# Kernel optimization log

Hardware: AMD Instinct MI355X
Metric: run time of the kernel (lower is better)

## Reference

```python
import jax, jax.numpy as jnp
import numpy as np

H = 256   # hidden_dim
S = 16    # d_state
B = 2
N = 8192
LN_EPS = 1e-5


def setup_inputs() -> dict:
    key = jax.random.key(0)
    ks = jax.random.split(key, 12)
    std = 1.0 / np.sqrt(H)
    inp = {
        'x': jax.random.normal(ks[0], (B, N, H), dtype=jnp.float32),
        'in_w': jax.random.normal(ks[1], (2 * H, H), dtype=jnp.float32) * std,
        'in_b': jax.random.normal(ks[2], (2 * H,), dtype=jnp.float32) * std,
        'xp_w': jax.random.normal(ks[3], (2 * S + 1, H), dtype=jnp.float32) * std,
        'xp_b': jax.random.normal(ks[4], (2 * S + 1,), dtype=jnp.float32) * std,
        'dt_w': jax.random.normal(ks[5], (H, 1), dtype=jnp.float32),
        'dt_b': jax.random.normal(ks[6], (H,), dtype=jnp.float32),
        'A_log': jnp.log(jnp.broadcast_to(jnp.arange(1, S + 1, dtype=jnp.float32), (H, S))),
        'D': jnp.ones((H,), dtype=jnp.float32),
        'out_w': jax.random.normal(ks[7], (H, H), dtype=jnp.float32) * std,
        'out_b': jax.random.normal(ks[8], (H,), dtype=jnp.float32) * std,
        'ln_g': jnp.ones((H,), dtype=jnp.float32),
        'ln_b': jnp.zeros((H,), dtype=jnp.float32),
    }
    return inp


def reference(x, in_w, in_b, xp_w, xp_b, dt_w, dt_b, A_log, D, out_w, out_b, ln_g, ln_b):
    # x: (B, N, H). Dropout is identity in eval mode.
    residual = x
    xz = jnp.einsum('bnh,kh->bnk', x, in_w) + in_b            # (B,N,2H)
    x_inner, z = xz[..., :H], xz[..., H:]
    x_dbl = jnp.einsum('bnh,kh->bnk', x_inner, xp_w) + xp_b   # (B,N,2S+1)
    dt_raw = x_dbl[..., :1]
    B_raw = x_dbl[..., 1:S + 1]                               # (B,N,S)
    C_raw = x_dbl[..., S + 1:]                                # (B,N,S)
    dt = jax.nn.softplus(dt_raw * dt_w[:, 0] + dt_b)          # (B,N,H)
    # NOTE: the original computes dA = exp(dt * A) but never uses it; A_log
    # does not affect the output, so we skip materializing dA.
    dB = dt[..., None] * B_raw[:, :, None, :]                 # (B,N,H,S)
    h = jnp.cumsum(x_inner[..., None] * dB, axis=1)           # (B,N,H,S)
    y = jnp.einsum('bnhs,bns->bnh', h, C_raw) + D * x_inner   # (B,N,H)
    y = y * jax.nn.silu(z)
    out = jnp.einsum('bnh,kh->bnk', y, out_w) + out_b
    r = out + residual
    mu = jnp.mean(r, axis=-1, keepdims=True)
    var = jnp.mean((r - mu) ** 2, axis=-1, keepdims=True)
    return ln_g * (r - mu) * jax.lax.rsqrt(var + LN_EPS) + ln_b
```

## Files before the change

### kernel.cpp

```cpp
#include <hip/hip_runtime.h>
#include <hip/hip_bf16.h>


#define HD 256
#define SD 16
#define NSEQ 8192
#define NBATCH 2
#define BN (NBATCH * NSEQ)
#define CHUNK 32
#define NCHUNK (NSEQ / CHUNK)
#define NGRP 16
#define GSZ (NCHUNK / NGRP)
#define LN_EPS 1e-5f
#define UST 40
#define PST 257

#define NX  (BN * HD)
#define NIW (2 * HD * HD)
#define NXP (48 * HD)
#define NOW (HD * HD)

typedef __hip_bfloat16 bf16;
typedef __attribute__((ext_vector_type(8))) short bf16x8;
typedef __attribute__((ext_vector_type(4))) short short4v;
typedef __attribute__((ext_vector_type(4))) float f32x4;
typedef __attribute__((ext_vector_type(4))) unsigned int uint4v;
typedef __attribute__((ext_vector_type(2))) unsigned int uint2v;

__device__ __forceinline__ float b2f(bf16 v) { return __bfloat162float(v); }
__device__ __forceinline__ short f2bs(float f) {
  union { bf16 b; short s; } u;
  u.b = __float2bfloat16(f);
  return u.s;
}
__device__ __forceinline__ unsigned int pack2(float a, float b) {
  return (unsigned int)(unsigned short)f2bs(a) |
         ((unsigned int)(unsigned short)f2bs(b) << 16);
}
__device__ __forceinline__ bf16x8 cvt_frag(const float* p) {
  bf16x8 r;
#pragma unroll
  for (int j = 0; j < 8; ++j) r[j] = f2bs(p[j]);
  return r;
}
__device__ __forceinline__ float softplus_f(float a) {
  return (a > 20.f) ? a : __logf(1.f + __expf(a));
}

__global__ __launch_bounds__(256) void k0_convert(
    const float* __restrict__ x, const float* __restrict__ in_w,
    const float* __restrict__ xp_w, const float* __restrict__ out_w,
    bf16* __restrict__ xb, bf16* __restrict__ wbin,
    bf16* __restrict__ wbxp, bf16* __restrict__ wbout)
{
  const int base = (blockIdx.x * 256 + threadIdx.x) * 4;
  if (base < NX) {
    f32x4 v = *(const f32x4*)(x + base);
    *(short4v*)((short*)xb + base) =
        short4v{f2bs(v[0]), f2bs(v[1]), f2bs(v[2]), f2bs(v[3])};
  } else if (base < NX + NIW) {
    const int off = base - NX;
    f32x4 v = *(const f32x4*)(in_w + off);
    *(short4v*)((short*)wbin + off) =
        short4v{f2bs(v[0]), f2bs(v[1]), f2bs(v[2]), f2bs(v[3])};
  } else if (base < NX + NIW + NXP) {
    const int off = base - NX - NIW;
    short4v s;
    if (off < 33 * HD) {
      f32x4 v = *(const f32x4*)(xp_w + off);
      s = short4v{f2bs(v[0]), f2bs(v[1]), f2bs(v[2]), f2bs(v[3])};
    } else {
      s = short4v{0, 0, 0, 0};
    }
    *(short4v*)((short*)wbxp + off) = s;
  } else if (base < NX + NIW + NXP + NOW) {
    const int off = base - NX - NIW - NXP;
    f32x4 v = *(const f32x4*)(out_w + off);
    *(short4v*)((short*)wbout + off) =
        short4v{f2bs(v[0]), f2bs(v[1]), f2bs(v[2]), f2bs(v[3])};
  }
}

__global__ __launch_bounds__(256) void k1_gemm(
    const bf16* __restrict__ xb, const bf16* __restrict__ wbin,
    const float* __restrict__ in_b, bf16* __restrict__ xib,
    bf16* __restrict__ zb)
{
  __shared__ __align__(16) char smem[128 * 264 * 2];
  bf16* Bt = (bf16*)smem;
  float* Ct = (float*)smem;

  const int tid = threadIdx.x;
  const int rt = blockIdx.x >> 2, ct = blockIdx.x & 3;
  const int R0 = rt * 128, C0 = ct * 128;
  const int wave = tid >> 6, lane = tid & 63, q = lane >> 4, l16 = lane & 15;

#pragma unroll
  for (int it = 0; it < 16; ++it) {
    const int f = tid + it * 256;
    const int row = f >> 5, g = f & 31;
    bf16x8 v = *(const bf16x8*)(wbin + (size_t)(C0 + row) * HD + g * 8);
    *(bf16x8*)(Bt + row * 264 + g * 8) = v;
  }
  __syncthreads();

  const int rowHalf = (wave & 1) * 64;
  const int colHalf = (wave >> 1) * 64;
  f32x4 acc[4][4] = {};
  const bf16* ap = xb + (size_t)(R0 + rowHalf + l16) * HD + q * 8;
#pragma unroll
  for (int k = 0; k < HD; k += 32) {
    bf16x8 a[4], b[4];
#pragma unroll
    for (int i = 0; i < 4; ++i)
      a[i] = *(const bf16x8*)(ap + (size_t)i * 16 * HD + k);
#pragma unroll
    for (int j = 0; j < 4; ++j)
      b[j] = *(const bf16x8*)(Bt + (colHalf + j * 16 + l16) * 264 + k + q * 8);
#pragma unroll
    for (int i = 0; i < 4; ++i)
#pragma unroll
      for (int j = 0; j < 4; ++j)
        acc[i][j] = __builtin_amdgcn_mfma_f32_16x16x32_bf16(a[i], b[j], acc[i][j], 0, 0, 0);
  }
  __syncthreads();

#pragma unroll
  for (int j = 0; j < 4; ++j) {
    const int col = colHalf + j * 16 + l16;
    const float bias = in_b[C0 + col];
#pragma unroll
    for (int i = 0; i < 4; ++i)
#pragma unroll
      for (int r = 0; r < 4; ++r)
        Ct[(rowHalf + i * 16 + q * 4 + r) * 132 + col] = acc[i][j][r] + bias;
  }
  __syncthreads();

  bf16* dst = (C0 < HD) ? xib : zb;
  const int Cd = (C0 < HD) ? C0 : (C0 - HD);
#pragma unroll
  for (int it = 0; it < 8; ++it) {
    const int f = tid + it * 256;
    const int row = f >> 4, g = f & 15;
    bf16x8 v = cvt_frag(Ct + row * 132 + g * 8);
    *(bf16x8*)(dst + (size_t)(R0 + row) * HD + Cd + g * 8) = v;
  }
}

__global__ __launch_bounds__(256) void kS_xp_sum(
    const bf16* __restrict__ xib, const bf16* __restrict__ wbxp,
    const float* __restrict__ xp_b, const float* __restrict__ dt_w,
    const float* __restrict__ dt_b, float* __restrict__ dbc,
    float* __restrict__ Mc)
{
  __shared__ __align__(16) bf16 xt[32 * 264];
  __shared__ __align__(16) bf16 wp[48 * 264];
  __shared__ __align__(16) float sdbc[32][33];
  __shared__ __align__(16) bf16 sBt[16 * UST];
  __shared__ __align__(16) bf16 Ut[256 * UST];
  const int tid = threadIdx.x;
  const int wave = tid >> 6, lane = tid & 63, q = lane >> 4, l16 = lane & 15;
  const int cix = blockIdx.x;
  const int R0 = cix * CHUNK;

#pragma unroll
  for (int it = 0; it < 4; ++it) {
    const int f = tid + it * 256, row = f >> 5, g = f & 31;
    *(bf16x8*)(xt + row * 264 + g * 8) =
        *(const bf16x8*)(xib + (size_t)(R0 + row) * HD + g * 8);
  }
#pragma unroll
  for (int it = 0; it < 6; ++it) {
    const int f = tid + it * 256, row = f >> 5, g = f & 31;
    *(bf16x8*)(wp + row * 264 + g * 8) =
        *(const bf16x8*)(wbxp + (size_t)row * HD + g * 8);
  }
  __syncthreads();

  if (wave < 2) {
    f32x4 pacc[3] = {};
#pragma unroll
    for (int k = 0; k < HD; k += 32) {
      bf16x8 af = *(const bf16x8*)(xt + (wave * 16 + l16) * 264 + k + q * 8);
#pragma unroll
      for (int t = 0; t < 3; ++t) {
        bf16x8 bfr = *(const bf16x8*)(wp + (t * 16 + l16) * 264 + k + q * 8);
        pacc[t] = __builtin_amdgcn_mfma_f32_16x16x32_bf16(af, bfr, pacc[t], 0, 0, 0);
      }
    }
#pragma unroll
    for (int t = 0; t < 3; ++t) {
      const int col = t * 16 + l16;
      if (col < 33) {
        const float bias = xp_b[col];
#pragma unroll
        for (int r = 0; r < 4; ++r) {
          const int row = wave * 16 + q * 4 + r;
          const float v = pacc[t][r] + bias;
          sdbc[row][col] = v;
          if (col >= 1 && col < 17)
            *((short*)sBt + (col - 1) * UST + row) = f2bs(v);
        }
      }
    }
  }
  __syncthreads();

  {
    const float* sflat = &sdbc[0][0];
    for (int idx = tid; idx < CHUNK * 33; idx += 256)
      dbc[(size_t)R0 * 33 + idx] = sflat[idx];
  }
  {
    const int h = tid;
    const float dtw = dt_w[h], dtb = dt_b[h];
    unsigned int up[16];
#pragma unroll
    for (int n2 = 0; n2 < 16; ++n2) {
      const int n = 2 * n2;
      const float xv0 = b2f(xt[n * 264 + h]);
      const float xv1 = b2f(xt[(n + 1) * 264 + h]);
      const float u0 = xv0 * softplus_f(sdbc[n][0] * dtw + dtb);
      const float u1 = xv1 * softplus_f(sdbc[n + 1][0] * dtw + dtb);
      up[n2] = pack2(u0, u1);
    }
    uint4v* dst = (uint4v*)(Ut + h * UST);
#pragma unroll
    for (int j = 0; j < 4; ++j)
      dst[j] = uint4v{up[4 * j], up[4 * j + 1], up[4 * j + 2], up[4 * j + 3]};
  }
  __syncthreads();

  {
    bf16x8 af = *(const bf16x8*)(sBt + l16 * UST + q * 8);
    f32x4 macc[4] = {};
#pragma unroll
    for (int c4 = 0; c4 < 4; ++c4) {
      const int ct = wave * 4 + c4;
      bf16x8 bu = *(const bf16x8*)(Ut + (ct * 16 + l16) * UST + q * 8);
      macc[c4] = __builtin_amdgcn_mfma_f32_16x16x32_bf16(af, bu, macc[c4], 0, 0, 0);
    }
    float* mbase = Mc + (size_t)cix * 4096;
#pragma unroll
    for (int c4 = 0; c4 < 4; ++c4) {
      const int h = (wave * 4 + c4) * 16 + l16;
#pragma unroll
      for (int r = 0; r < 4; ++r)
        mbase[(q * 4 + r) * HD + h] = macc[c4][r];
    }
  }
}

__global__ __launch_bounds__(256) void k4a_prefix_local(
    float* __restrict__ Mc, float* __restrict__ Gs)
{
  const int tid = blockIdx.x * 256 + threadIdx.x;
  const int b = tid >> 16;
  const int g = (tid >> 12) & (NGRP - 1);
  const int hs = tid & 4095;
  float run = 0.f;
#pragma unroll
  for (int i = 0; i < GSZ; ++i) {
    const size_t idx = ((size_t)(b * NCHUNK + g * GSZ + i)) * 4096 + hs;
    const float v = Mc[idx];
    Mc[idx] = run;
    run += v;
  }
  Gs[((size_t)(b * NGRP + g)) * 4096 + hs] = run;
}

__global__ __launch_bounds__(256) void k4b_prefix_groups(float* __restrict__ Gs)
{
  const int tid = blockIdx.x * 256 + threadIdx.x;
  const int b = tid >> 12;
  const int hs = tid & 4095;
  float run = 0.f;
#pragma unroll
  for (int g = 0; g < NGRP; ++g) {
    const size_t idx = ((size_t)(b * NGRP + g)) * 4096 + hs;
    const float v = Gs[idx];
    Gs[idx] = run;
    run += v;
  }
}

__global__ __launch_bounds__(256) void k56_scan_out_ln(
    const bf16* __restrict__ xib, const bf16* __restrict__ zb,
    const float* __restrict__ dbc, const float* __restrict__ dt_w,
    const float* __restrict__ dt_b, const float* __restrict__ Dv,
    const float* __restrict__ Mc, const float* __restrict__ Gs,
    const bf16* __restrict__ wbout, const float* __restrict__ out_b,
    const float* __restrict__ x, const float* __restrict__ ln_g,
    const float* __restrict__ ln_b, float* __restrict__ out)
{
  __shared__ __align__(16) char un[53376];
  bf16* Ut  = (bf16*)un;
  bf16* Hst = (bf16*)(un + 20480);
  bf16* Ctl = (bf16*)(un + 40960);
  bf16* Tt  = (bf16*)(un + 43520);
  bf16* yb  = (bf16*)un;
  float* pt = (float*)(un + 20480);
  __shared__ float sdbc[32][33];

  const int tid = threadIdx.x;
  const int wave = tid >> 6, lane = tid & 63, q = lane >> 4, l16 = lane & 15;
  const int cix = blockIdx.x;
  const int R0 = cix * CHUNK;
  const int b = cix >> 8;
  const int cchunk = cix & 255;

  {
    float* sflat = &sdbc[0][0];
    for (int idx = tid; idx < CHUNK * 33; idx += 256)
      sflat[idx] = dbc[(size_t)R0 * 33 + idx];
  }
  __syncthreads();

  {
    const int n = tid >> 3;
    const int m0 = (tid & 7) * 4;
    float cn[SD];
#pragma unroll
    for (int s = 0; s < SD; ++s) cn[s] = sdbc[n][17 + s];
    short4v tv;
#pragma unroll
    for (int mm = 0; mm < 4; ++mm) {
      const int m = m0 + mm;
      float t = 0.f;
#pragma unroll
      for (int s = 0; s < SD; ++s) t += cn[s] * sdbc[m][1 + s];
      tv[mm] = (m <= n) ? f2bs(t) : (short)0;
    }
    *(short4v*)((short*)Tt + n * 32 + m0) = tv;
  }
  {
    const int n = tid >> 3, k0 = (tid & 7) * 4;
    float v[4];
#pragma unroll
    for (int j = 0; j < 4; ++j) {
      const int k = k0 + j;
      v[j] = (k < SD) ? sdbc[n][17 + k] : 0.f;
    }
    *(uint2v*)((short*)Ctl + n * UST + k0) = uint2v{pack2(v[0], v[1]), pack2(v[2], v[3])};
  }
  {
    const int h = tid;
    const float* mp = Mc + (size_t)cix * 4096 + h;
    const float* gp = Gs + ((size_t)(b * NGRP + cchunk / GSZ)) * 4096 + h;
    unsigned int hp[8];
#pragma unroll
    for (int s2 = 0; s2 < 8; ++s2) {
      const int s = 2 * s2;
      const float v0 = mp[s * HD] + gp[s * HD];
      const float v1 = mp[(s + 1) * HD] + gp[(s + 1) * HD];
      hp[s2] = pack2(v0, v1);
    }
    uint4v* hd = (uint4v*)(Hst + h * UST);
    hd[0] = uint4v{hp[0], hp[1], hp[2], hp[3]};
    hd[1] = uint4v{hp[4], hp[5], hp[6], hp[7]};
    hd[2] = uint4v{0, 0, 0, 0};
    hd[3] = uint4v{0, 0, 0, 0};
  }
  {
    const int h = tid;
    const float dtw = dt_w[h], dtb = dt_b[h];
    unsigned int up[16];
#pragma unroll
    for (int n2 = 0; n2 < 16; ++n2) {
      const int n = 2 * n2;
      const float xv0 = b2f(xib[(size_t)(R0 + n) * HD + h]);
      const float xv1 = b2f(xib[(size_t)(R0 + n + 1) * HD + h]);
      const float u0 = xv0 * softplus_f(sdbc[n][0] * dtw + dtb);
      const float u1 = xv1 * softplus_f(sdbc[n + 1][0] * dtw + dtb);
      up[n2] = pack2(u0, u1);
    }
    uint4v* dst = (uint4v*)(Ut + h * UST);
#pragma unroll
    for (int j = 0; j < 4; ++j)
      dst[j] = uint4v{up[4 * j], up[4 * j + 1], up[4 * j + 2], up[4 * j + 3]};
  }
  __syncthreads();

  f32x4 acc[2][4] = {};
  {
    bf16x8 aT0 = *(const bf16x8*)(Tt + l16 * 32 + q * 8);
    bf16x8 aT1 = *(const bf16x8*)(Tt + (16 + l16) * 32 + q * 8);
    bf16x8 aC0 = *(const bf16x8*)(Ctl + l16 * UST + q * 8);
    bf16x8 aC1 = *(const bf16x8*)(Ctl + (16 + l16) * UST + q * 8);
#pragma unroll
    for (int c4 = 0; c4 < 4; ++c4) {
      const int ct = wave * 4 + c4;
      bf16x8 bu = *(const bf16x8*)(Ut + (ct * 16 + l16) * UST + q * 8);
      bf16x8 bh = *(const bf16x8*)(Hst + (ct * 16 + l16) * UST + q * 8);
      acc[0][c4] = __builtin_amdgcn_mfma_f32_16x16x32_bf16(aT0, bu, acc[0][c4], 0, 0, 0);
      acc[0][c4] = __builtin_amdgcn_mfma_f32_16x16x32_bf16(aC0, bh, acc[0][c4], 0, 0, 0);
      acc[1][c4] = __builtin_amdgcn_mfma_f32_16x16x32_bf16(aT1, bu, acc[1][c4], 0, 0, 0);
      acc[1][c4] = __builtin_amdgcn_mfma_f32_16x16x32_bf16(aC1, bh, acc[1][c4], 0, 0, 0);
    }
  }
  __syncthreads();

  {
#pragma unroll
    for (int c4 = 0; c4 < 4; ++c4) {
      const int h = (wave * 4 + c4) * 16 + l16;
      const float dh = Dv[h];
#pragma unroll
      for (int rt = 0; rt < 2; ++rt)
#pragma unroll
        for (int r = 0; r < 4; ++r) {
          const int n = rt * 16 + q * 4 + r;
          const size_t grow = (size_t)(R0 + n) * HD + h;
          const float xv = b2f(xib[grow]);
          const float zv = b2f(zb[grow]);
          const float yv = acc[rt][c4][r] + dh * xv;
          const float sig = 1.f / (1.f + __expf(-zv));
          ((short*)yb)[n * 264 + h] = f2bs(yv * zv * sig);
        }
    }
  }
  __syncthreads();

  const int cw = wave * 64;
  f32x4 oacc[2][4] = {};
#pragma unroll
  for (int k = 0; k < HD; k += 32) {
    bf16x8 a0 = *(const bf16x8*)(yb + l16 * 264 + k + q * 8);
    bf16x8 a1 = *(const bf16x8*)(yb + (16 + l16) * 264 + k + q * 8);
#pragma unroll
    for (int t = 0; t < 4; ++t) {
      bf16x8 bfr = *(const bf16x8*)(wbout + (size_t)(cw + t * 16 + l16) * HD + k + q * 8);
      oacc[0][t] = __builtin_amdgcn_mfma_f32_16x16x32_bf16(a0, bfr, oacc[0][t], 0, 0, 0);
      oacc[1][t] = __builtin_amdgcn_mfma_f32_16x16x32_bf16(a1, bfr, oacc[1][t], 0, 0, 0);
    }
  }
#pragma unroll
  for (int t = 0; t < 4; ++t) {
    const int col = cw + t * 16 + l16;
    const float bias = out_b[col];
#pragma unroll
    for (int rt = 0; rt < 2; ++rt)
#pragma unroll
      for (int r = 0; r < 4; ++r) {
        const int row = rt * 16 + q * 4 + r;
        pt[row * PST + col] = oacc[rt][t][r] + bias + x[(size_t)(R0 + row) * HD + col];
      }
  }
  __syncthreads();

#pragma unroll
  for (int rr = 0; rr < 8; ++rr) {
    const int row = wave * 8 + rr;
    float p = 0.f;
#pragma unroll
    for (int j = 0; j < 4; ++j) p += pt[row * PST + lane + 64 * j];
#pragma unroll
    for (int off = 32; off > 0; off >>= 1) p += __shfl_xor(p, off);
    const float mu = p * (1.f / 256.f);
    float v2 = 0.f;
#pragma unroll
    for (int j = 0; j < 4; ++j) {
      const float d = pt[row * PST + lane + 64 * j] - mu;
      v2 += d * d;
    }
#pragma unroll
    for (int off = 32; off > 0; off >>= 1) v2 += __shfl_xor(v2, off);
    const float rstd = rsqrtf(v2 * (1.f / 256.f) + LN_EPS);
    const size_t base = (size_t)(R0 + row) * HD;
#pragma unroll
    for (int j = 0; j < 4; ++j) {
      const int cc = lane + 64 * j;
      out[base + cc] = ln_g[cc] * (pt[row * PST + cc] - mu) * rstd + ln_b[cc];
    }
  }
}

extern "C" void kernel_launch(void* const* d_in, const int* in_sizes, int n_in,
                              void* d_out, int out_size, void* d_ws, size_t ws_size,
                              hipStream_t stream)
{
  const float* x     = (const float*)d_in[0];
  const float* in_w  = (const float*)d_in[1];
  const float* in_b  = (const float*)d_in[2];
  const float* xp_w  = (const float*)d_in[3];
  const float* xp_b  = (const float*)d_in[4];
  const float* dt_w  = (const float*)d_in[5];
  const float* dt_b  = (const float*)d_in[6];
  const float* Dv    = (const float*)d_in[8];
  const float* out_w = (const float*)d_in[9];
  const float* out_b = (const float*)d_in[10];
  const float* ln_g  = (const float*)d_in[11];
  const float* ln_b  = (const float*)d_in[12];

  char* ws = (char*)d_ws;
  bf16*  xib   = (bf16*)(ws);
  bf16*  zb    = (bf16*)(ws +  8388608);
  bf16*  xb    = (bf16*)(ws + 16777216);
  float* dbc   = (float*)(ws + 25165824);
  float* Mc    = (float*)(ws + 27328512);
  float* Gs    = (float*)(ws + 35717120);
  bf16*  wbin  = (bf16*)(ws + 36241408);
  bf16*  wbxp  = (bf16*)(ws + 36503552);
  bf16*  wbout = (bf16*)(ws + 36528128);
  float* out   = (float*)d_out;

  hipLaunchKernelGGL(k0_convert, dim3((NX + NIW + NXP + NOW) / 1024), dim3(256),
                     0, stream, x, in_w, xp_w, out_w, xb, wbin, wbxp, wbout);
  hipLaunchKernelGGL(k1_gemm, dim3(512), dim3(256), 0, stream,
                     xb, wbin, in_b, xib, zb);
  hipLaunchKernelGGL(kS_xp_sum, dim3(BN / CHUNK), dim3(256), 0, stream,
                     xib, wbxp, xp_b, dt_w, dt_b, dbc, Mc);
  hipLaunchKernelGGL(k4a_prefix_local, dim3(NBATCH * NGRP * 4096 / 256),
                     dim3(256), 0, stream, Mc, Gs);
  hipLaunchKernelGGL(k4b_prefix_groups, dim3(NBATCH * 4096 / 256), dim3(256),
                     0, stream, Gs);
  hipLaunchKernelGGL(k56_scan_out_ln, dim3(BN / CHUNK), dim3(256), 0, stream,
                     xib, zb, dbc, dt_w, dt_b, Dv, Mc, Gs,
                     wbout, out_b, x, ln_g, ln_b, out);
}
```

Measured before the change: 143.2 us.

## Fuse x fp32-to-bf16 conversion into input GEMM, staging x tile in LDS

The separate pass that converted all of x to bf16 in workspace is removed; the input-projection GEMM now loads its 128-row x tile from fp32, converts it in registers and stores it to LDS. Weights are read directly from global as the B operand, and the block index mapping is swapped so consecutive blocks share a column tile of weights. This removes a full read and write of x in bf16 plus the extra traffic, but x tiles are now converted by each of the four column-tile blocks (4x redundant conversion and fp32 reads of x).

```diff
diff --git a/kernel.cpp b/kernel.cpp
--- a/kernel.cpp
+++ b/kernel.cpp
@@ -15,7 +15,6 @@
 #define UST 40
 #define PST 257
 
-#define NX  (BN * HD)
 #define NIW (2 * HD * HD)
 #define NXP (48 * HD)
 #define NOW (HD * HD)
@@ -47,24 +46,18 @@
   return (a > 20.f) ? a : __logf(1.f + __expf(a));
 }
 
-__global__ __launch_bounds__(256) void k0_convert(
-    const float* __restrict__ x, const float* __restrict__ in_w,
-    const float* __restrict__ xp_w, const float* __restrict__ out_w,
-    bf16* __restrict__ xb, bf16* __restrict__ wbin,
+__global__ __launch_bounds__(256) void k0_weights(
+    const float* __restrict__ in_w, const float* __restrict__ xp_w,
+    const float* __restrict__ out_w, bf16* __restrict__ wbin,
     bf16* __restrict__ wbxp, bf16* __restrict__ wbout)
 {
   const int base = (blockIdx.x * 256 + threadIdx.x) * 4;
-  if (base < NX) {
-    f32x4 v = *(const f32x4*)(x + base);
-    *(short4v*)((short*)xb + base) =
+  if (base < NIW) {
+    f32x4 v = *(const f32x4*)(in_w + base);
+    *(short4v*)((short*)wbin + base) =
         short4v{f2bs(v[0]), f2bs(v[1]), f2bs(v[2]), f2bs(v[3])};
-  } else if (base < NX + NIW) {
-    const int off = base - NX;
-    f32x4 v = *(const f32x4*)(in_w + off);
-    *(short4v*)((short*)wbin + off) =
-        short4v{f2bs(v[0]), f2bs(v[1]), f2bs(v[2]), f2bs(v[3])};
-  } else if (base < NX + NIW + NXP) {
-    const int off = base - NX - NIW;
+  } else if (base < NIW + NXP) {
+    const int off = base - NIW;
     short4v s;
     if (off < 33 * HD) {
       f32x4 v = *(const f32x4*)(xp_w + off);
@@ -73,8 +66,8 @@
       s = short4v{0, 0, 0, 0};
     }
     *(short4v*)((short*)wbxp + off) = s;
-  } else if (base < NX + NIW + NXP + NOW) {
-    const int off = base - NX - NIW - NXP;
+  } else if (base < NIW + NXP + NOW) {
+    const int off = base - NIW - NXP;
     f32x4 v = *(const f32x4*)(out_w + off);
     *(short4v*)((short*)wbout + off) =
         short4v{f2bs(v[0]), f2bs(v[1]), f2bs(v[2]), f2bs(v[3])};
@@ -82,16 +75,16 @@
 }
 
 __global__ __launch_bounds__(256) void k1_gemm(
-    const bf16* __restrict__ xb, const bf16* __restrict__ wbin,
+    const float* __restrict__ x, const bf16* __restrict__ wbin,
     const float* __restrict__ in_b, bf16* __restrict__ xib,
     bf16* __restrict__ zb)
 {
   __shared__ __align__(16) char smem[128 * 264 * 2];
-  bf16* Bt = (bf16*)smem;
+  bf16* At = (bf16*)smem;
   float* Ct = (float*)smem;
 
   const int tid = threadIdx.x;
-  const int rt = blockIdx.x >> 2, ct = blockIdx.x & 3;
+  const int rt = blockIdx.x & 127, ct = blockIdx.x >> 7;
   const int R0 = rt * 128, C0 = ct * 128;
   const int wave = tid >> 6, lane = tid & 63, q = lane >> 4, l16 = lane & 15;
 
@@ -99,24 +92,24 @@
   for (int it = 0; it < 16; ++it) {
     const int f = tid + it * 256;
     const int row = f >> 5, g = f & 31;
-    bf16x8 v = *(const bf16x8*)(wbin + (size_t)(C0 + row) * HD + g * 8);
-    *(bf16x8*)(Bt + row * 264 + g * 8) = v;
+    bf16x8 v = cvt_frag(x + (size_t)(R0 + row) * HD + g * 8);
+    *(bf16x8*)(At + row * 264 + g * 8) = v;
   }
   __syncthreads();
 
   const int rowHalf = (wave & 1) * 64;
   const int colHalf = (wave >> 1) * 64;
   f32x4 acc[4][4] = {};
-  const bf16* ap = xb + (size_t)(R0 + rowHalf + l16) * HD + q * 8;
+  const bf16* bp = wbin + (size_t)(C0 + colHalf + l16) * HD + q * 8;
 #pragma unroll
   for (int k = 0; k < HD; k += 32) {
     bf16x8 a[4], b[4];
 #pragma unroll
     for (int i = 0; i < 4; ++i)
-      a[i] = *(const bf16x8*)(ap + (size_t)i * 16 * HD + k);
+      a[i] = *(const bf16x8*)(At + (rowHalf + i * 16 + l16) * 264 + k + q * 8);
 #pragma unroll
     for (int j = 0; j < 4; ++j)
-      b[j] = *(const bf16x8*)(Bt + (colHalf + j * 16 + l16) * 264 + k + q * 8);
+      b[j] = *(const bf16x8*)(bp + (size_t)j * 16 * HD + k);
 #pragma unroll
     for (int i = 0; i < 4; ++i)
 #pragma unroll
@@ -352,9 +345,7 @@
 #pragma unroll
     for (int s2 = 0; s2 < 8; ++s2) {
       const int s = 2 * s2;
-      const float v0 = mp[s * HD] + gp[s * HD];
-      const float v1 = mp[(s + 1) * HD] + gp[(s + 1) * HD];
-      hp[s2] = pack2(v0, v1);
+      hp[s2] = pack2(mp[s * HD] + gp[s * HD], mp[(s + 1) * HD] + gp[(s + 1) * HD]);
     }
     uint4v* hd = (uint4v*)(Hst + h * UST);
     hd[0] = uint4v{hp[0], hp[1], hp[2], hp[3]};
@@ -496,19 +487,18 @@
   char* ws = (char*)d_ws;
   bf16*  xib   = (bf16*)(ws);
   bf16*  zb    = (bf16*)(ws +  8388608);
-  bf16*  xb    = (bf16*)(ws + 16777216);
-  float* dbc   = (float*)(ws + 25165824);
-  float* Mc    = (float*)(ws + 27328512);
-  float* Gs    = (float*)(ws + 35717120);
-  bf16*  wbin  = (bf16*)(ws + 36241408);
-  bf16*  wbxp  = (bf16*)(ws + 36503552);
-  bf16*  wbout = (bf16*)(ws + 36528128);
+  float* dbc   = (float*)(ws + 16777216);
+  float* Mc    = (float*)(ws + 18939904);
+  float* Gs    = (float*)(ws + 27328512);
+  bf16*  wbin  = (bf16*)(ws + 27852800);
+  bf16*  wbxp  = (bf16*)(ws + 28114944);
+  bf16*  wbout = (bf16*)(ws + 28139520);
   float* out   = (float*)d_out;
 
-  hipLaunchKernelGGL(k0_convert, dim3((NX + NIW + NXP + NOW) / 1024), dim3(256),
-                     0, stream, x, in_w, xp_w, out_w, xb, wbin, wbxp, wbout);
+  hipLaunchKernelGGL(k0_weights, dim3((NIW + NXP + NOW) / 1024), dim3(256),
+                     0, stream, in_w, xp_w, out_w, wbin, wbxp, wbout);
   hipLaunchKernelGGL(k1_gemm, dim3(512), dim3(256), 0, stream,
-                     xb, wbin, in_b, xib, zb);
+                     x, wbin, in_b, xib, zb);
   hipLaunchKernelGGL(kS_xp_sum, dim3(BN / CHUNK), dim3(256), 0, stream,
                      xib, wbxp, xp_b, dt_w, dt_b, dbc, Mc);
   hipLaunchKernelGGL(k4a_prefix_local, dim3(NBATCH * NGRP * 4096 / 256),
```

Result: no change. 142.1 us (-0.8%).
